# Kernel optimization log

Measured on AMD Instinct MI355X. Metric: run time of the kernel, lower is better.

The kernel has to match this reference:

```python
import jax, jax.numpy as jnp
import numpy as np

V = 32000   # vocab_size
D = 512     # d_model == d_hidden
B = 8       # batch
T = 512     # seq_len
N_LAYERS = 2


def setup_inputs() -> dict:
    key = jax.random.key(0)
    ks = jax.random.split(key, 10)
    tokens = jax.random.randint(ks[0], (B, T), 0, V, dtype=jnp.int32)
    embed = jax.random.normal(ks[1], (V, D), dtype=jnp.float32)  # stddev=1.0 init
    s = 1.0 / np.sqrt(D)
    # per-layer LSTM params: Wx [D,4D], Wh [D,4D], b [4D] (gate order i,f,g,o)
    Wx0 = jax.random.normal(ks[2], (D, 4 * D), dtype=jnp.float32) * s
    Wh0 = jax.random.normal(ks[3], (D, 4 * D), dtype=jnp.float32) * s
    b0 = jnp.zeros((4 * D,), dtype=jnp.float32)
    Wx1 = jax.random.normal(ks[4], (D, 4 * D), dtype=jnp.float32) * s
    Wh1 = jax.random.normal(ks[5], (D, 4 * D), dtype=jnp.float32) * s
    b1 = jnp.zeros((4 * D,), dtype=jnp.float32)
    Wout = jax.random.normal(ks[6], (D, V), dtype=jnp.float32) * s
    bout = jnp.zeros((V,), dtype=jnp.float32)
    return {"tokens": tokens, "embed": embed,
            "Wx0": Wx0, "Wh0": Wh0, "b0": b0,
            "Wx1": Wx1, "Wh1": Wh1, "b1": b1,
            "Wout": Wout, "bout": bout}


def _lstm_layer(x, Wx, Wh, b):
    # x: [B, T, D] -> h_seq: [B, T, D]
    # Precompute input contribution for all timesteps (one big GEMM).
    xW = jnp.einsum('btd,dh->bth', x, Wx) + b  # [B, T, 4D]
    xW_t = jnp.swapaxes(xW, 0, 1)              # [T, B, 4D]
    h0 = jnp.zeros((x.shape[0], Wh.shape[0]), dtype=x.dtype)
    c0 = jnp.zeros_like(h0)

    def step(carry, xw):
        h, c = carry
        gates = xw + h @ Wh                    # [B, 4D]
        i, f, g, o = jnp.split(gates, 4, axis=-1)
        i = jax.nn.sigmoid(i)
        f = jax.nn.sigmoid(f)
        g = jnp.tanh(g)
        o = jax.nn.sigmoid(o)
        c_new = f * c + i * g
        h_new = o * jnp.tanh(c_new)
        return (h_new, c_new), h_new

    _, h_seq = jax.lax.scan(step, (h0, c0), xW_t)  # [T, B, D]
    return jnp.swapaxes(h_seq, 0, 1)


def reference(tokens, embed, Wx0, Wh0, b0, Wx1, Wh1, b1, Wout, bout):
    # ShiftRight(axis=1): prepend zero token, drop last.
    shifted = jnp.pad(tokens, ((0, 0), (1, 0)))[:, :-1]
    x = embed[shifted]                         # [B, T, D]
    x = _lstm_layer(x, Wx0, Wh0, b0)
    x = _lstm_layer(x, Wx1, Wh1, b1)
    # Dropout with deterministic=True is the identity.
    logits = jnp.einsum('btd,dv->btv', x, Wout) + bout  # [B, T, V]
    return logits
```

## Files before the change

kernel.cpp:

```cpp
#include <hip/hip_runtime.h>
#include <cstdint>


typedef float    f32x4  __attribute__((ext_vector_type(4)));
typedef __bf16   bf16x8 __attribute__((ext_vector_type(8)));
typedef uint16_t u16;

constexpr int BB = 8, T = 512, D = 512, V = 32000;
constexpr int M4 = BB * T;
constexpr int G  = 4 * D;

static __device__ __forceinline__ u16 f2bf(float f) {
  union { float f; uint32_t u; } v{f};
  uint32_t r = v.u + 0x7fffu + ((v.u >> 16) & 1u);
  return (u16)(r >> 16);
}
static __device__ __forceinline__ float sigm(float x)  { return 1.f / (1.f + __expf(-x)); }
static __device__ __forceinline__ float tanhr(float x) { return 1.f - 2.f / (__expf(2.f * x) + 1.f); }

__global__ void embed_kernel(const int* __restrict__ tok, const float* __restrict__ emb,
                             u16* __restrict__ Xbf) {
  int m = blockIdx.x;
  int b = m >> 9, t = m & 511;
  int id = t ? tok[b * T + t - 1] : 0;
  const float* src = emb + (size_t)id * D;
  u16* dst = Xbf + (size_t)m * D;
  for (int d = threadIdx.x; d < D; d += 256) dst[d] = f2bf(src[d]);
}

template <bool PERM>
__global__ void transpose_cast(const float* __restrict__ src, u16* __restrict__ dst, int Cn) {
  __shared__ float tl[64][65];
  int n0 = blockIdx.x * 64, k0 = blockIdx.y * 64;
  int tx = threadIdx.x & 63, ty = threadIdx.x >> 6;
  for (int r = ty; r < 64; r += 4) tl[r][tx] = src[(size_t)(k0 + r) * Cn + n0 + tx];
  __syncthreads();
  for (int r = ty; r < 64; r += 4) {
    int n = n0 + r;
    int q = PERM ? ((n & (D - 1)) * 4 + (n >> 9)) : n;
    dst[(size_t)q * D + k0 + tx] = f2bf(tl[tx][r]);
  }
}

__global__ void bias_perm(const float* __restrict__ b, float* __restrict__ bp) {
  int q = blockIdx.x * 256 + threadIdx.x;
  if (q < G) bp[q] = b[(q & 3) * D + (q >> 2)];
}

__global__ __launch_bounds__(256) void gemm_bt(
    const u16* __restrict__ A, const u16* __restrict__ BT,
    const float* __restrict__ bias, float* __restrict__ C, int N, int K) {
  __shared__ u16 As[128 * 32], Bs[128 * 32];
  const int lane = threadIdx.x & 63, wave = threadIdx.x >> 6;
  const int m0 = blockIdx.y * 128, n0 = blockIdx.x * 128;
  const int wm = (wave >> 1) * 64, wn = (wave & 1) * 64;
  const int lr = lane >> 2, lc = (lane & 3) * 8;
  f32x4 acc[4][4] = {};
  for (int kk = 0; kk < K; kk += 32) {
#pragma unroll
    for (int i = 0; i < 2; ++i) {
      int row = wave * 32 + i * 16;
      __builtin_amdgcn_global_load_lds(
          (const __attribute__((address_space(1))) uint32_t*)(A + (size_t)(m0 + row + lr) * K + kk + lc),
          (__attribute__((address_space(3))) uint32_t*)(As + row * 32), 16, 0, 0);
      __builtin_amdgcn_global_load_lds(
          (const __attribute__((address_space(1))) uint32_t*)(BT + (size_t)(n0 + row + lr) * K + kk + lc),
          (__attribute__((address_space(3))) uint32_t*)(Bs + row * 32), 16, 0, 0);
    }
    __syncthreads();
    bf16x8 af[4], bf[4];
#pragma unroll
    for (int i = 0; i < 4; ++i) {
      af[i] = *(const bf16x8*)(As + (wm + i * 16 + (lane & 15)) * 32 + (lane >> 4) * 8);
      bf[i] = *(const bf16x8*)(Bs + (wn + i * 16 + (lane & 15)) * 32 + (lane >> 4) * 8);
    }
#pragma unroll
    for (int mi = 0; mi < 4; ++mi)
#pragma unroll
      for (int ni = 0; ni < 4; ++ni)
        acc[mi][ni] = __builtin_amdgcn_mfma_f32_16x16x32_bf16(af[mi], bf[ni], acc[mi][ni], 0, 0, 0);
    __syncthreads();
  }
  const int cr = (lane >> 4) * 4, cc = lane & 15;
#pragma unroll
  for (int ni = 0; ni < 4; ++ni) {
    int col = n0 + wn + ni * 16 + cc;
    float bv = bias[col];
#pragma unroll
    for (int mi = 0; mi < 4; ++mi) {
      size_t base = (size_t)(m0 + wm + mi * 16 + cr) * N + col;
#pragma unroll
      for (int r = 0; r < 4; ++r) C[base + (size_t)r * N] = acc[mi][ni][r] + bv;
    }
  }
}

__global__ __launch_bounds__(256) void lstm_scan(
    const u16* __restrict__ WhT, const float* __restrict__ xw,
    u16* __restrict__ Hstep, u16* __restrict__ Hseq, int* __restrict__ flags) {
  __shared__ u16 Wlds[64 * 512];
  __shared__ float Cst[4][16][16];
  const int tid = threadIdx.x, lane = tid & 63, wave = tid >> 6, wg = blockIdx.x;
  {
    const uint4* s = (const uint4*)(WhT + (size_t)wg * 64 * 512);
    uint4* dsh = (uint4*)Wlds;
    for (int i = tid; i < 64 * 512 / 8; i += 256) dsh[i] = s[i];
  }
  __syncthreads();
  const int fr = lane & 15, quad = lane >> 4;
  const int colbase = wave * 16;
  const bool gl = lane < 32;
  const int b = lane & 7, dl = (lane >> 3) & 3;
  const int dglob = wg * 16 + wave * 4 + dl;
  const int q16 = wg * 64 + wave * 16;
  float c_state = 0.f;
  for (int t = 0; t < T; ++t) {
    const u16* hr = Hstep + (size_t)(t & 1) * (16 * 512);
    f32x4 acc0 = {}, acc1 = {};
#pragma unroll
    for (int kb = 0; kb < 16; kb += 2) {
      bf16x8 a0 = *(const bf16x8*)(hr + fr * 512 + kb * 32 + quad * 8);
      bf16x8 w0 = *(const bf16x8*)(Wlds + (colbase + fr) * 512 + kb * 32 + quad * 8);
      acc0 = __builtin_amdgcn_mfma_f32_16x16x32_bf16(a0, w0, acc0, 0, 0, 0);
      bf16x8 a1 = *(const bf16x8*)(hr + fr * 512 + (kb + 1) * 32 + quad * 8);
      bf16x8 w1 = *(const bf16x8*)(Wlds + (colbase + fr) * 512 + (kb + 1) * 32 + quad * 8);
      acc1 = __builtin_amdgcn_mfma_f32_16x16x32_bf16(a1, w1, acc1, 0, 0, 0);
    }
    f32x4 acc = acc0 + acc1;
#pragma unroll
    for (int r = 0; r < 4; ++r) Cst[wave][quad * 4 + r][fr] = acc[r];
    __syncthreads();
    if (gl) {
      const float4 x4 = *(const float4*)(xw + (size_t)(b * T + t) * G + q16 + dl * 4);
      float pi = Cst[wave][b][dl * 4 + 0] + x4.x;
      float pf = Cst[wave][b][dl * 4 + 1] + x4.y;
      float pg = Cst[wave][b][dl * 4 + 2] + x4.z;
      float po = Cst[wave][b][dl * 4 + 3] + x4.w;
      float ig = sigm(pi), fg = sigm(pf), gg = tanhr(pg), og = sigm(po);
      c_state = fg * c_state + ig * gg;
      float h = og * tanhr(c_state);
      u16 hb = f2bf(h);
      Hstep[(size_t)((t + 1) & 1) * (16 * 512) + b * 512 + dglob] = hb;
      Hseq[(size_t)(b * T + t) * 512 + dglob] = hb;
    }
    __syncthreads();
    if (wave == 0) {
      if (lane == 0)
        __hip_atomic_store(&flags[wg], t + 1, __ATOMIC_RELEASE, __HIP_MEMORY_SCOPE_AGENT);
      for (;;) {
        int v = (lane < 32) ? __hip_atomic_load(&flags[lane], __ATOMIC_ACQUIRE, __HIP_MEMORY_SCOPE_AGENT)
                            : t + 1;
        if (__all(v >= t + 1)) break;
        __builtin_amdgcn_s_sleep(1);
      }
    }
    __syncthreads();
  }
}

extern "C" void kernel_launch(void* const* d_in, const int* in_sizes, int n_in,
                              void* d_out, int out_size, void* d_ws, size_t ws_size,
                              hipStream_t stream) {
  (void)in_sizes; (void)n_in; (void)out_size; (void)ws_size;
  const int*   tokens = (const int*)d_in[0];
  const float* embed  = (const float*)d_in[1];
  const float* Wx0 = (const float*)d_in[2];
  const float* Wh0 = (const float*)d_in[3];
  const float* b0  = (const float*)d_in[4];
  const float* Wx1 = (const float*)d_in[5];
  const float* Wh1 = (const float*)d_in[6];
  const float* b1  = (const float*)d_in[7];
  const float* Wout = (const float*)d_in[8];
  const float* bout = (const float*)d_in[9];

  char* ws = (char*)d_ws;
  size_t off = 0;
  auto alloc = [&](size_t bytes) -> char* {
    char* p = ws + off; off += (bytes + 255) & ~(size_t)255; return p;
  };
  float* xw  = (float*)alloc((size_t)M4 * G * 4);
  u16* WoutT = (u16*)xw;
  u16* Xbf   = (u16*)alloc((size_t)M4 * D * 2);
  u16* WxT0  = (u16*)alloc((size_t)G * D * 2);
  u16* WhT0  = (u16*)alloc((size_t)G * D * 2);
  u16* WxT1  = (u16*)alloc((size_t)G * D * 2);
  u16* WhT1  = (u16*)alloc((size_t)G * D * 2);
  u16* Hbf0  = (u16*)alloc((size_t)M4 * D * 2);
  u16* Hbf1  = (u16*)alloc((size_t)M4 * D * 2);
  float* b0p = (float*)alloc(G * 4);
  float* b1p = (float*)alloc(G * 4);
  char* zbase = ws + off;
  u16* Hstep0 = (u16*)alloc(2 * 16 * 512 * 2);
  u16* Hstep1 = (u16*)alloc(2 * 16 * 512 * 2);
  int* flags0 = (int*)alloc(256);
  int* flags1 = (int*)alloc(256);
  size_t zbytes = (size_t)((ws + off) - zbase);
  hipMemsetAsync(zbase, 0, zbytes, stream);

  embed_kernel<<<M4, 256, 0, stream>>>(tokens, embed, Xbf);
  transpose_cast<true ><<<dim3(G / 64, 8), 256, 0, stream>>>(Wx0, WxT0, G);
  transpose_cast<true ><<<dim3(G / 64, 8), 256, 0, stream>>>(Wh0, WhT0, G);
  transpose_cast<true ><<<dim3(G / 64, 8), 256, 0, stream>>>(Wx1, WxT1, G);
  transpose_cast<true ><<<dim3(G / 64, 8), 256, 0, stream>>>(Wh1, WhT1, G);
  bias_perm<<<G / 256, 256, 0, stream>>>(b0, b0p);
  bias_perm<<<G / 256, 256, 0, stream>>>(b1, b1p);

  gemm_bt<<<dim3(G / 128, M4 / 128), 256, 0, stream>>>(Xbf, WxT0, b0p, xw, G, D);
  lstm_scan<<<32, 256, 0, stream>>>(WhT0, xw, Hstep0, Hbf0, flags0);
  gemm_bt<<<dim3(G / 128, M4 / 128), 256, 0, stream>>>(Hbf0, WxT1, b1p, xw, G, D);
  lstm_scan<<<32, 256, 0, stream>>>(WhT1, xw, Hstep1, Hbf1, flags1);
  transpose_cast<false><<<dim3(V / 64, 8), 256, 0, stream>>>(Wout, WoutT, V);
  gemm_bt<<<dim3(V / 128, M4 / 128), 256, 0, stream>>>(Hbf1, WoutT, bout, (float*)d_out, V, D);
}
```

Baseline: 6.124 ms.

## Fuse both LSTM layers into one wavefront-pipelined persistent kernel

Replaces the two sequential per-layer scan kernels and the layer-1 input GEMM with one 64-workgroup kernel. Layer-0 workgroups run one step ahead of layer-1 workgroups, and layer 1 computes its input projection per step from the layer-0 hidden ring. Weights move from LDS into registers, flags are padded to avoid false sharing, and the per-step barrier is replaced by per-lane flag polling. This overlaps the two serial recurrences and drops one GEMM plus the intermediate hidden-sequence buffer, at the cost of more register pressure, doubled MFMA work per layer-1 step, and cross-layer synchronisation.

```diff
diff --git a/kernel.cpp b/kernel.cpp
--- a/kernel.cpp
+++ b/kernel.cpp
@@ -9,6 +9,7 @@
 constexpr int BB = 8, T = 512, D = 512, V = 32000;
 constexpr int M4 = BB * T;
 constexpr int G  = 4 * D;
+constexpr int FS = 16;
 
 static __device__ __forceinline__ u16 f2bf(float f) {
   union { float f; uint32_t u; } v{f};
@@ -95,66 +96,121 @@
   }
 }
 
-__global__ __launch_bounds__(256) void lstm_scan(
-    const u16* __restrict__ WhT, const float* __restrict__ xw,
-    u16* __restrict__ Hstep, u16* __restrict__ Hseq, int* __restrict__ flags) {
-  __shared__ u16 Wlds[64 * 512];
+__global__ __launch_bounds__(256, 1) void lstm_fused(
+    const u16* __restrict__ WhT0, const u16* __restrict__ WhT1, const u16* __restrict__ WxT1,
+    const float* __restrict__ xw0, const float* __restrict__ b1p,
+    u16* __restrict__ H0ring, u16* __restrict__ H1ring, u16* __restrict__ Hseq1,
+    int* __restrict__ flags) {
   __shared__ float Cst[4][16][16];
   const int tid = threadIdx.x, lane = tid & 63, wave = tid >> 6, wg = blockIdx.x;
-  {
-    const uint4* s = (const uint4*)(WhT + (size_t)wg * 64 * 512);
-    uint4* dsh = (uint4*)Wlds;
-    for (int i = tid; i < 64 * 512 / 8; i += 256) dsh[i] = s[i];
-  }
-  __syncthreads();
+  const bool L1 = wg >= 32;
+  const int wgl = L1 ? wg - 32 : wg;
+  const int q16 = wgl * 64 + wave * 16;
   const int fr = lane & 15, quad = lane >> 4;
-  const int colbase = wave * 16;
   const bool gl = lane < 32;
   const int b = lane & 7, dl = (lane >> 3) & 3;
-  const int dglob = wg * 16 + wave * 4 + dl;
-  const int q16 = wg * 64 + wave * 16;
-  float c_state = 0.f;
-  for (int t = 0; t < T; ++t) {
-    const u16* hr = Hstep + (size_t)(t & 1) * (16 * 512);
-    f32x4 acc0 = {}, acc1 = {};
-#pragma unroll
-    for (int kb = 0; kb < 16; kb += 2) {
-      bf16x8 a0 = *(const bf16x8*)(hr + fr * 512 + kb * 32 + quad * 8);
-      bf16x8 w0 = *(const bf16x8*)(Wlds + (colbase + fr) * 512 + kb * 32 + quad * 8);
-      acc0 = __builtin_amdgcn_mfma_f32_16x16x32_bf16(a0, w0, acc0, 0, 0, 0);
-      bf16x8 a1 = *(const bf16x8*)(hr + fr * 512 + (kb + 1) * 32 + quad * 8);
-      bf16x8 w1 = *(const bf16x8*)(Wlds + (colbase + fr) * 512 + (kb + 1) * 32 + quad * 8);
-      acc1 = __builtin_amdgcn_mfma_f32_16x16x32_bf16(a1, w1, acc1, 0, 0, 0);
-    }
-    f32x4 acc = acc0 + acc1;
-#pragma unroll
-    for (int r = 0; r < 4; ++r) Cst[wave][quad * 4 + r][fr] = acc[r];
-    __syncthreads();
-    if (gl) {
-      const float4 x4 = *(const float4*)(xw + (size_t)(b * T + t) * G + q16 + dl * 4);
-      float pi = Cst[wave][b][dl * 4 + 0] + x4.x;
-      float pf = Cst[wave][b][dl * 4 + 1] + x4.y;
-      float pg = Cst[wave][b][dl * 4 + 2] + x4.z;
-      float po = Cst[wave][b][dl * 4 + 3] + x4.w;
-      float ig = sigm(pi), fg = sigm(pf), gg = tanhr(pg), og = sigm(po);
-      c_state = fg * c_state + ig * gg;
-      float h = og * tanhr(c_state);
-      u16 hb = f2bf(h);
-      Hstep[(size_t)((t + 1) & 1) * (16 * 512) + b * 512 + dglob] = hb;
-      Hseq[(size_t)(b * T + t) * 512 + dglob] = hb;
-    }
-    __syncthreads();
-    if (wave == 0) {
-      if (lane == 0)
-        __hip_atomic_store(&flags[wg], t + 1, __ATOMIC_RELEASE, __HIP_MEMORY_SCOPE_AGENT);
+  const int dbase = wgl * 16 + wave * 4;
+
+  if (!L1) {
+    bf16x8 whf[16];
+#pragma unroll
+    for (int kb = 0; kb < 16; ++kb)
+      whf[kb] = *(const bf16x8*)(WhT0 + (size_t)(q16 + fr) * 512 + kb * 32 + quad * 8);
+    float c_state = 0.f;
+    for (int t = 0; t < T; ++t) {
+      const int thr = t - ((lane >= 32) ? 1 : 0);
       for (;;) {
-        int v = (lane < 32) ? __hip_atomic_load(&flags[lane], __ATOMIC_ACQUIRE, __HIP_MEMORY_SCOPE_AGENT)
-                            : t + 1;
-        if (__all(v >= t + 1)) break;
+        int v = __hip_atomic_load(&flags[lane * FS], __ATOMIC_ACQUIRE, __HIP_MEMORY_SCOPE_AGENT);
+        if (__all(v >= thr)) break;
         __builtin_amdgcn_s_sleep(1);
       }
-    }
-    __syncthreads();
+      float4 x4 = *(const float4*)(xw0 + (size_t)(b * T + t) * G + q16 + dl * 4);
+      const u16* hA = H0ring + ((t & 1) ^ 1) * 8192;
+      f32x4 acc0 = {}, acc1 = {};
+#pragma unroll
+      for (int kb = 0; kb < 16; kb += 2) {
+        bf16x8 a0 = *(const bf16x8*)(hA + fr * 512 + kb * 32 + quad * 8);
+        acc0 = __builtin_amdgcn_mfma_f32_16x16x32_bf16(a0, whf[kb], acc0, 0, 0, 0);
+        bf16x8 a1 = *(const bf16x8*)(hA + fr * 512 + (kb + 1) * 32 + quad * 8);
+        acc1 = __builtin_amdgcn_mfma_f32_16x16x32_bf16(a1, whf[kb + 1], acc1, 0, 0, 0);
+      }
+      f32x4 acc = acc0 + acc1;
+#pragma unroll
+      for (int r = 0; r < 4; ++r) Cst[wave][quad * 4 + r][fr] = acc[r];
+      int hv = 0;
+      if (gl) {
+        float pi = Cst[wave][b][dl * 4 + 0] + x4.x;
+        float pf = Cst[wave][b][dl * 4 + 1] + x4.y;
+        float pg = Cst[wave][b][dl * 4 + 2] + x4.z;
+        float po = Cst[wave][b][dl * 4 + 3] + x4.w;
+        float ig = sigm(pi), fg = sigm(pf), gg = tanhr(pg), og = sigm(po);
+        c_state = fg * c_state + ig * gg;
+        hv = f2bf(og * tanhr(c_state));
+        int g0 = __shfl(hv, b + 0), g1 = __shfl(hv, b + 8);
+        int g2 = __shfl(hv, b + 16), g3 = __shfl(hv, b + 24);
+        if (lane < 8) {
+          ushort4 p = { (u16)g0, (u16)g1, (u16)g2, (u16)g3 };
+          *(ushort4*)(H0ring + (t & 1) * 8192 + b * 512 + dbase) = p;
+        }
+      }
+      __syncthreads();
+      if (tid == 0)
+        __hip_atomic_store(&flags[wg * FS], t + 1, __ATOMIC_RELEASE, __HIP_MEMORY_SCOPE_AGENT);
+    }
+  } else {
+    bf16x8 whf[16], wxf[16];
+#pragma unroll
+    for (int kb = 0; kb < 16; ++kb) {
+      whf[kb] = *(const bf16x8*)(WhT1 + (size_t)(q16 + fr) * 512 + kb * 32 + quad * 8);
+      wxf[kb] = *(const bf16x8*)(WxT1 + (size_t)(q16 + fr) * 512 + kb * 32 + quad * 8);
+    }
+    float4 bias4 = *(const float4*)(b1p + q16 + dl * 4);
+    float c_state = 0.f;
+    for (int t = 0; t < T; ++t) {
+      const int thr = t + 1 - ((lane >= 32) ? 1 : 0);
+      for (;;) {
+        int v = __hip_atomic_load(&flags[lane * FS], __ATOMIC_ACQUIRE, __HIP_MEMORY_SCOPE_AGENT);
+        if (__all(v >= thr)) break;
+        __builtin_amdgcn_s_sleep(1);
+      }
+      const u16* hA0 = H0ring + (t & 1) * 8192;
+      const u16* hA1 = H1ring + ((t & 1) ^ 1) * 8192;
+      f32x4 acc0 = {}, acc1 = {}, acc2 = {}, acc3 = {};
+#pragma unroll
+      for (int kb = 0; kb < 16; kb += 2) {
+        bf16x8 a0 = *(const bf16x8*)(hA0 + fr * 512 + kb * 32 + quad * 8);
+        acc0 = __builtin_amdgcn_mfma_f32_16x16x32_bf16(a0, wxf[kb], acc0, 0, 0, 0);
+        bf16x8 a1 = *(const bf16x8*)(hA1 + fr * 512 + kb * 32 + quad * 8);
+        acc1 = __builtin_amdgcn_mfma_f32_16x16x32_bf16(a1, whf[kb], acc1, 0, 0, 0);
+        bf16x8 a2 = *(const bf16x8*)(hA0 + fr * 512 + (kb + 1) * 32 + quad * 8);
+        acc2 = __builtin_amdgcn_mfma_f32_16x16x32_bf16(a2, wxf[kb + 1], acc2, 0, 0, 0);
+        bf16x8 a3 = *(const bf16x8*)(hA1 + fr * 512 + (kb + 1) * 32 + quad * 8);
+        acc3 = __builtin_amdgcn_mfma_f32_16x16x32_bf16(a3, whf[kb + 1], acc3, 0, 0, 0);
+      }
+      f32x4 acc = (acc0 + acc1) + (acc2 + acc3);
+#pragma unroll
+      for (int r = 0; r < 4; ++r) Cst[wave][quad * 4 + r][fr] = acc[r];
+      int hv = 0; ushort4 p;
+      if (gl) {
+        float pi = Cst[wave][b][dl * 4 + 0] + bias4.x;
+        float pf = Cst[wave][b][dl * 4 + 1] + bias4.y;
+        float pg = Cst[wave][b][dl * 4 + 2] + bias4.z;
+        float po = Cst[wave][b][dl * 4 + 3] + bias4.w;
+        float ig = sigm(pi), fg = sigm(pf), gg = tanhr(pg), og = sigm(po);
+        c_state = fg * c_state + ig * gg;
+        hv = f2bf(og * tanhr(c_state));
+        int g0 = __shfl(hv, b + 0), g1 = __shfl(hv, b + 8);
+        int g2 = __shfl(hv, b + 16), g3 = __shfl(hv, b + 24);
+        p = { (u16)g0, (u16)g1, (u16)g2, (u16)g3 };
+        if (lane < 8)
+          *(ushort4*)(H1ring + (t & 1) * 8192 + b * 512 + dbase) = p;
+      }
+      __syncthreads();
+      if (tid == 0)
+        __hip_atomic_store(&flags[wg * FS], t + 1, __ATOMIC_RELEASE, __HIP_MEMORY_SCOPE_AGENT);
+      if (gl && lane < 8)
+        *(ushort4*)(Hseq1 + (size_t)(b * T + t) * 512 + dbase) = p;
+    }
   }
 }
 
@@ -185,15 +241,13 @@
   u16* WhT0  = (u16*)alloc((size_t)G * D * 2);
   u16* WxT1  = (u16*)alloc((size_t)G * D * 2);
   u16* WhT1  = (u16*)alloc((size_t)G * D * 2);
-  u16* Hbf0  = (u16*)alloc((size_t)M4 * D * 2);
-  u16* Hbf1  = (u16*)alloc((size_t)M4 * D * 2);
+  u16* Hseq1 = (u16*)alloc((size_t)M4 * D * 2);
   float* b0p = (float*)alloc(G * 4);
   float* b1p = (float*)alloc(G * 4);
   char* zbase = ws + off;
-  u16* Hstep0 = (u16*)alloc(2 * 16 * 512 * 2);
-  u16* Hstep1 = (u16*)alloc(2 * 16 * 512 * 2);
-  int* flags0 = (int*)alloc(256);
-  int* flags1 = (int*)alloc(256);
+  u16* H0ring = (u16*)alloc(2 * 16 * 512 * 2);
+  u16* H1ring = (u16*)alloc(2 * 16 * 512 * 2);
+  int* flags  = (int*)alloc(64 * FS * 4);
   size_t zbytes = (size_t)((ws + off) - zbase);
   hipMemsetAsync(zbase, 0, zbytes, stream);
 
@@ -206,9 +260,7 @@
   bias_perm<<<G / 256, 256, 0, stream>>>(b1, b1p);
 
   gemm_bt<<<dim3(G / 128, M4 / 128), 256, 0, stream>>>(Xbf, WxT0, b0p, xw, G, D);
-  lstm_scan<<<32, 256, 0, stream>>>(WhT0, xw, Hstep0, Hbf0, flags0);
-  gemm_bt<<<dim3(G / 128, M4 / 128), 256, 0, stream>>>(Hbf0, WxT1, b1p, xw, G, D);
-  lstm_scan<<<32, 256, 0, stream>>>(WhT1, xw, Hstep1, Hbf1, flags1);
+  lstm_fused<<<64, 256, 0, stream>>>(WhT0, WhT1, WxT1, xw, b1p, H0ring, H1ring, Hseq1, flags);
   transpose_cast<false><<<dim3(V / 64, 8), 256, 0, stream>>>(Wout, WoutT, V);
-  gemm_bt<<<dim3(V / 128, M4 / 128), 256, 0, stream>>>(Hbf1, WoutT, bout, (float*)d_out, V, D);
-}
+  gemm_bt<<<dim3(V / 128, M4 / 128), 256, 0, stream>>>(Hseq1, WoutT, bout, (float*)d_out, V, D);
+}
```

After: 5.630 ms. -8.1%, faster.
